# Performance work log

Hardware: AMD Instinct MI355X
Metric: run time of the kernel (lower is better)

Reference implementation:

```python
import jax, jax.numpy as jnp
import numpy as np


def setup_inputs() -> dict:
    key = jax.random.key(0)
    hidden_states = jax.random.normal(key, (8, 4096, 768), dtype=jnp.float32)
    return {"hidden_states": hidden_states}


def reference(hidden_states) -> jnp.ndarray:
    # fft along seq dim (-2), then along hidden dim (-1), keep real part.
    # Equivalent to a 2D FFT over the last two axes.
    x = hidden_states.astype(jnp.float32)
    out = jnp.fft.fft(jnp.fft.fft(x, axis=-2), axis=-1).real
    return out.astype(hidden_states.dtype)
```

## Files before the change

kernel.cpp:

```cpp
#include <hip/hip_runtime.h>
#include <hip/hip_bf16.h>

#define N1 4096
#define N2 768
#define NCC 384
#define WS_NEEDED 100663296ull
#define WS1_UINTS 12582912ull

__device__ __forceinline__ float2 cadd(float2 a, float2 b){ return make_float2(a.x+b.x, a.y+b.y); }
__device__ __forceinline__ float2 csub(float2 a, float2 b){ return make_float2(a.x-b.x, a.y-b.y); }
__device__ __forceinline__ float2 cmul(float2 a, float2 b){ return make_float2(a.x*b.x - a.y*b.y, a.x*b.y + a.y*b.x); }
__device__ __forceinline__ float2 cnegi(float2 a){ return make_float2(a.y, -a.x); }

__device__ __forceinline__ unsigned pack_bf2(float2 v) {
  unsigned ax = __float_as_uint(v.x); ax = (ax + 0x7FFFu + ((ax >> 16) & 1u)) >> 16;
  unsigned ay = __float_as_uint(v.y); ay = (ay + 0x7FFFu + ((ay >> 16) & 1u)) & 0xFFFF0000u;
  return ax | ay;
}
__device__ __forceinline__ float2 unpack_bf2(unsigned u) {
  return make_float2(__uint_as_float(u << 16), __uint_as_float(u & 0xFFFF0000u));
}
__device__ __forceinline__ float bf2f(unsigned short u) {
  return __uint_as_float((unsigned)u << 16);
}

__device__ __forceinline__ int rev6(int p) {
  int k = 0;
  #pragma unroll
  for (int i = 0; i < 6; ++i) { k = (k << 2) | (p & 3); p >>= 2; }
  return k;
}

__device__ __forceinline__ void fft8(float2 z[8]) {
  const float RH = 0.70710678118654752f;
  float2 u0=cadd(z[0],z[4]), v0=csub(z[0],z[4]);
  float2 u1=cadd(z[1],z[5]), v1=csub(z[1],z[5]);
  float2 u2=cadd(z[2],z[6]), v2=csub(z[2],z[6]);
  float2 u3=cadd(z[3],z[7]), v3=csub(z[3],z[7]);
  v1 = make_float2(RH*(v1.x+v1.y), RH*(v1.y-v1.x));
  v2 = cnegi(v2);
  v3 = make_float2(RH*(v3.y-v3.x), -RH*(v3.x+v3.y));
  float2 a0=cadd(u0,u2), b0=csub(u0,u2);
  float2 a1=cadd(u1,u3), b1=cnegi(csub(u1,u3));
  float2 c0=cadd(v0,v2), d0=csub(v0,v2);
  float2 c1=cadd(v1,v3), d1=cnegi(csub(v1,v3));
  z[0]=cadd(a0,a1); z[4]=csub(a0,a1);
  z[2]=cadd(b0,b1); z[6]=csub(b0,b1);
  z[1]=cadd(c0,c1); z[5]=csub(c0,c1);
  z[3]=cadd(d0,d1); z[7]=csub(d0,d1);
}

__global__ __launch_bounds__(1024) void p1a_kernel(const float* __restrict__ x,
                                                   unsigned* __restrict__ ws1) {
  __shared__ float4 S4[64*65];
  float2* S = reinterpret_cast<float2*>(S4);
  int bid = blockIdx.x;
  int b8  = bid & 7;
  int rem = bid >> 3;
  int cg  = rem / 64;
  int a   = rem % 64;
  const int t = threadIdx.x, l = t & 63, w = t >> 6;

  const float* src = x + (size_t)b8 * N1 * N2 + (size_t)cg * 256;
  #pragma unroll
  for (int j = 0; j < 4; ++j) {
    int r   = 4*w + j;
    int row = a + 64*r;
    S4[r*65 + l] = *reinterpret_cast<const float4*>(src + (size_t)row * N2 + 4*l);
  }
  __syncthreads();

  const int c = t & 127, b0 = t >> 7;
  float2 z[8];
  #pragma unroll
  for (int b1 = 0; b1 < 8; ++b1) z[b1] = S[(8*b1 + b0)*130 + c];
  fft8(z);
  {
    float sn, cs; __sincosf(-6.283185307179586f/64.f * (float)b0, &sn, &cs);
    float2 wstep = make_float2(cs, sn), wcur = wstep;
    #pragma unroll
    for (int j = 1; j < 8; ++j) { z[j] = cmul(z[j], wcur); wcur = cmul(wcur, wstep); }
  }
  __syncthreads();
  #pragma unroll
  for (int j = 0; j < 8; ++j) S[(j*8 + b0)*130 + c] = z[j];
  __syncthreads();

  const int jj = t >> 7;
  #pragma unroll
  for (int b0i = 0; b0i < 8; ++b0i) z[b0i] = S[(jj*8 + b0i)*130 + c];
  fft8(z);
  float2 wc, w8;
  { float sn, cs; __sincosf(-6.283185307179586f/4096.f * (float)(a*jj), &sn, &cs); wc = make_float2(cs, sn); }
  { float sn, cs; __sincosf(-6.283185307179586f/4096.f * (float)(8*a),  &sn, &cs); w8 = make_float2(cs, sn); }
  unsigned* wdst = ws1 + (((size_t)b8*64 + a)*3 + cg)*8192 + (size_t)jj*128 + c;
  #pragma unroll
  for (int m = 0; m < 8; ++m) {
    wdst[(size_t)m * 1024] = pack_bf2(cmul(z[m], wc));
    wc = cmul(wc, w8);
  }
}

__global__ __launch_bounds__(1024) void p1b_kernel(const unsigned* __restrict__ ws1,
                                                   unsigned* __restrict__ ws2) {
  __shared__ float2 T[2][4096];
  int bid = blockIdx.x;
  int b8  = bid & 7;
  int rem = bid >> 3;
  int cg  = rem / 32, kbt = rem % 32;
  int kb0 = (kbt == 0) ? 0  : kbt;
  int kb1 = (kbt == 0) ? 32 : 64 - kbt;
  const int t = threadIdx.x, l = t & 63, wv = (t >> 6) & 7, ti = t >> 9;
  const int kb = ti ? kb1 : kb0;
  const int cgA = cg >> 1, chalf = (cg & 1) * 64;

  const unsigned* wsrc = ws1 + ((size_t)b8*64*3 + cgA)*8192
                             + (size_t)kb*128 + chalf + l;
  float2 z[8];
  #pragma unroll
  for (int a1 = 0; a1 < 8; ++a1)
    z[a1] = unpack_bf2(wsrc[(size_t)(8*a1 + wv) * 24576]);
  fft8(z);
  float fac = -6.283185307179586f/64.0f * (float)wv;
  #pragma unroll
  for (int q = 1; q < 8; ++q) {
    float sn, cs; __sincosf(fac * (float)q, &sn, &cs);
    z[q] = cmul(z[q], make_float2(cs, sn));
  }
  #pragma unroll
  for (int q = 0; q < 8; ++q) T[ti][(q*8 + wv)*64 + l] = z[q];
  __syncthreads();
  #pragma unroll
  for (int a0 = 0; a0 < 8; ++a0) z[a0] = T[ti][(wv*8 + a0)*64 + l];
  fft8(z);
  __syncthreads();
  #pragma unroll
  for (int ka1 = 0; ka1 < 8; ++ka1) T[ti][(8*ka1 + wv)*64 + l] = z[ka1];
  __syncthreads();

  unsigned* wout = ws2 + (size_t)b8 * N1 * NCC + (size_t)cg*64 + l;
  #pragma unroll
  for (int it = 0; it < 8; ++it) {
    int ka = 8*it + wv;
    int tj, kap;
    if (kbt == 0) { tj = ti; kap = ti ? (63 - ka) : ((64 - ka) & 63); }
    else          { tj = 1 - ti; kap = 63 - ka; }
    float2 Zk = T[ti][ka*64 + l];
    float2 Zp = T[tj][kap*64 + l];
    int r = kb + 64*ka;
    float2 o;
    if (r <= 2048) o = make_float2(0.5f*(Zk.x + Zp.x), 0.5f*(Zk.y + Zp.y));
    else           o = make_float2(0.5f*(Zp.y - Zk.y), 0.5f*(Zk.x - Zp.x));
    wout[(size_t)r * NCC] = pack_bf2(o);
  }
}

__global__ __launch_bounds__(256) void fft_hid_bf16(const unsigned* __restrict__ ws2,
                                                    float* __restrict__ out) {
  __shared__ float T[4][12*69];
  const int grp = threadIdx.x >> 6;
  const int l   = threadIdx.x & 63;
  int task = blockIdx.x * 4 + grp;
  int b  = task / 2049;
  int t1 = task - b * 2049;
  const bool special = (t1 == 0) || (t1 == 2048);
  const int mrow = special ? t1 : (N1 - t1);
  const unsigned short* pre16 = (const unsigned short*)ws2 + ((size_t)b*N1 + t1)*N2;
  const unsigned short* pim16 = (const unsigned short*)ws2 + ((size_t)b*N1 + mrow)*N2;

  float2 z[12];
  #pragma unroll
  for (int m = 0; m < 12; ++m) {
    float re = bf2f(pre16[(m << 6) + l]);
    float im = special ? 0.0f : bf2f(pim16[(m << 6) + l]);
    z[m] = make_float2(re, im);
  }

  float2 A[3][4];
  #pragma unroll
  for (int q = 0; q < 3; ++q) {
    float2 s0 = z[q], s1 = z[3+q], s2 = z[6+q], s3 = z[9+q];
    float2 t0 = cadd(s0,s2), t1v = csub(s0,s2);
    float2 t2 = cadd(s1,s3), t3 = cnegi(csub(s1,s3));
    A[q][0] = cadd(t0,t2); A[q][1] = cadd(t1v,t3);
    A[q][2] = csub(t0,t2); A[q][3] = csub(t1v,t3);
  }
  const float h3 = 0.8660254037844386f;
  const float2 W1[4] = { {1.f,0.f}, {h3,-0.5f}, {0.5f,-h3}, {0.f,-1.f} };
  const float2 W2[4] = { {1.f,0.f}, {0.5f,-h3}, {-0.5f,-h3}, {-1.f,0.f} };
  float2 y[12];
  #pragma unroll
  for (int k4 = 0; k4 < 4; ++k4) {
    float2 C0 = A[0][k4];
    float2 C1 = cmul(A[1][k4], W1[k4]);
    float2 C2 = cmul(A[2][k4], W2[k4]);
    float2 tt = cadd(C1,C2), d = csub(C1,C2);
    float2 u  = make_float2(C0.x - 0.5f*tt.x, C0.y - 0.5f*tt.y);
    float2 idd = make_float2(h3*d.y, -h3*d.x);
    y[k4]   = cadd(C0, tt);
    y[k4+4] = cadd(u, idd);
    y[k4+8] = csub(u, idd);
  }

  float base = -6.283185307179586f * (float)l / 768.0f;
  #pragma unroll
  for (int km = 1; km < 12; ++km) {
    float sn, cs; __sincosf(base * (float)km, &sn, &cs);
    y[km] = cmul(y[km], make_float2(cs, sn));
  }

  #pragma unroll
  for (int st = 0; st < 6; ++st) {
    int h = 32 >> st;
    int j = l & (h - 1);
    float sn, cs; __sincosf(-3.14159265358979f * (float)j / (float)h, &sn, &cs);
    float2 w = make_float2(cs, sn);
    bool hi = (l & h) != 0;
    #pragma unroll
    for (int m = 0; m < 12; ++m) {
      float px = __shfl_xor(y[m].x, h, 64);
      float py = __shfl_xor(y[m].y, h, 64);
      float2 p = make_float2(px, py);
      float2 lo  = cadd(y[m], p);
      float2 hiv = cmul(csub(p, y[m]), w);
      y[m] = hi ? hiv : lo;
    }
  }

  int r = ((l&1)<<5)|((l&2)<<3)|((l&4)<<1)|((l&8)>>1)|((l&16)>>3)|((l&32)>>5);
  float* Tb = T[grp];
  #pragma unroll
  for (int km = 0; km < 12; ++km) Tb[km*69 + r] = y[km].x;
  __syncthreads();

  float* pre = out + ((size_t)b*N1 + t1)*N2;
  float* pim = out + ((size_t)b*N1 + mrow)*N2;
  #pragma unroll
  for (int mp = 0; mp < 12; ++mp) {
    int k = (mp << 6) + l;
    float v = Tb[(k % 12)*69 + (k / 12)];
    pre[k] = v;
    if (!special) pim[(N2 - k) % N2] = v;
  }
}

#define PADI(i) ((i) + ((i) >> 4))
#define CPBUF 4352

__device__ __forceinline__ void bfly4p(float2* arr, int base, int M, float fac, int np) {
  float2 a0 = arr[PADI(base)], a1 = arr[PADI(base+M)];
  float2 a2 = arr[PADI(base+2*M)], a3 = arr[PADI(base+3*M)];
  float2 t0 = cadd(a0,a2), t1 = csub(a0,a2);
  float2 t2 = cadd(a1,a3), t3 = cnegi(csub(a1,a3));
  float2 y0 = cadd(t0,t2), y1 = cadd(t1,t3), y2 = csub(t0,t2), y3 = csub(t1,t3);
  float ang = fac * (float)np;
  float sn, cs; __sincosf(ang, &sn, &cs);
  float2 w1 = make_float2(cs, sn);
  float2 w2 = cmul(w1,w1);
  float2 w3 = cmul(w2,w1);
  arr[PADI(base)]     = y0;
  arr[PADI(base+M)]   = cmul(y1,w1);
  arr[PADI(base+2*M)] = cmul(y2,w2);
  arr[PADI(base+3*M)] = cmul(y3,w3);
}

__global__ __launch_bounds__(1024) void fft_seq_fused(const float* __restrict__ x,
                                                      float* __restrict__ out) {
  extern __shared__ float2 lds[];
  int bid = blockIdx.x;
  int wg  = (bid & 7) * 96 + (bid >> 3);
  int b   = wg / 96;
  int g   = wg % 96;
  const int t = threadIdx.x;
  const size_t base = (size_t)b * N1 * N2 + 8 * (size_t)g;

  for (int r = t; r < N1; r += 1024) {
    const float* p = x + base + (size_t)r * N2;
    float4 A  = *reinterpret_cast<const float4*>(p);
    float4 Bv = *reinterpret_cast<const float4*>(p + 4);
    int ip = PADI(r);
    lds[ip]             = make_float2(A.x, A.y);
    lds[CPBUF + ip]     = make_float2(A.z, A.w);
    lds[2*CPBUF + ip]   = make_float2(Bv.x, Bv.y);
    lds[3*CPBUF + ip]   = make_float2(Bv.z, Bv.w);
  }
  __syncthreads();

  const int wv  = t >> 6;
  const int cp  = wv & 3;
  const int idx = ((wv >> 2) << 6) + (t & 63);
  float2* buf = lds + cp * CPBUF;

  #pragma unroll
  for (int s = 0; s < 6; ++s) {
    int lm = 10 - 2*s;
    int M  = 1 << lm;
    float fac = -6.283185307179586f / (float)(4*M);
    #pragma unroll
    for (int jj = 0; jj < 4; ++jj) {
      int j   = idx + (jj << 8);
      int np  = j & (M-1);
      int grp = j >> lm;
      int bse = (grp << (lm+2)) + np;
      bfly4p(buf, bse, M, fac, np);
    }
    __syncthreads();
  }

  float* orow = out + base;
  #pragma unroll
  for (int i = 0; i < 4; ++i) {
    int k  = ((t & 63) << 6) + (t >> 6) + (i << 4);
    int km = (N1 - k) & (N1 - 1);
    int pk = PADI(rev6(k));
    int pn = PADI(rev6(km));
    float o[8];
    #pragma unroll
    for (int c = 0; c < 4; ++c) {
      float2 zk = lds[c*CPBUF + pk];
      float2 zn = lds[c*CPBUF + pn];
      if (k <= 2048) { o[2*c] = 0.5f*(zk.x + zn.x); o[2*c+1] = 0.5f*(zk.y + zn.y); }
      else           { o[2*c] = 0.5f*(zn.y - zk.y); o[2*c+1] = 0.5f*(zk.x - zn.x); }
    }
    float* q = orow + (size_t)k * N2;
    *reinterpret_cast<float4*>(q)     = make_float4(o[0], o[1], o[2], o[3]);
    *reinterpret_cast<float4*>(q + 4) = make_float4(o[4], o[5], o[6], o[7]);
  }
}

__global__ __launch_bounds__(256) void fft_hid_f32(float* __restrict__ out) {
  __shared__ float T[4][12*69];
  const int grp = threadIdx.x >> 6;
  const int l   = threadIdx.x & 63;
  int task = blockIdx.x * 4 + grp;
  int b  = task / 2049;
  int t1 = task - b * 2049;
  const bool special = (t1 == 0) || (t1 == 2048);
  const int mrow = special ? t1 : (N1 - t1);
  float* baseB = out + (size_t)b * N1 * N2;
  float* pre = baseB + (size_t)t1 * N2;
  float* pim = baseB + (size_t)mrow * N2;

  float2 z[12];
  #pragma unroll
  for (int m = 0; m < 12; ++m) {
    float re = pre[(m << 6) + l];
    float im = special ? 0.0f : pim[(m << 6) + l];
    z[m] = make_float2(re, im);
  }

  float2 A[3][4];
  #pragma unroll
  for (int q = 0; q < 3; ++q) {
    float2 s0 = z[q], s1 = z[3+q], s2 = z[6+q], s3 = z[9+q];
    float2 t0 = cadd(s0,s2), t1v = csub(s0,s2);
    float2 t2 = cadd(s1,s3), t3 = cnegi(csub(s1,s3));
    A[q][0] = cadd(t0,t2); A[q][1] = cadd(t1v,t3);
    A[q][2] = csub(t0,t2); A[q][3] = csub(t1v,t3);
  }
  const float h3 = 0.8660254037844386f;
  const float2 W1[4] = { {1.f,0.f}, {h3,-0.5f}, {0.5f,-h3}, {0.f,-1.f} };
  const float2 W2[4] = { {1.f,0.f}, {0.5f,-h3}, {-0.5f,-h3}, {-1.f,0.f} };
  float2 y[12];
  #pragma unroll
  for (int k4 = 0; k4 < 4; ++k4) {
    float2 C0 = A[0][k4];
    float2 C1 = cmul(A[1][k4], W1[k4]);
    float2 C2 = cmul(A[2][k4], W2[k4]);
    float2 tt = cadd(C1,C2), d = csub(C1,C2);
    float2 u  = make_float2(C0.x - 0.5f*tt.x, C0.y - 0.5f*tt.y);
    float2 idd = make_float2(h3*d.y, -h3*d.x);
    y[k4]   = cadd(C0, tt);
    y[k4+4] = cadd(u, idd);
    y[k4+8] = csub(u, idd);
  }

  float base = -6.283185307179586f * (float)l / 768.0f;
  #pragma unroll
  for (int km = 1; km < 12; ++km) {
    float sn, cs; __sincosf(base * (float)km, &sn, &cs);
    y[km] = cmul(y[km], make_float2(cs, sn));
  }

  #pragma unroll
  for (int st = 0; st < 6; ++st) {
    int h = 32 >> st;
    int j = l & (h - 1);
    float sn, cs; __sincosf(-3.14159265358979f * (float)j / (float)h, &sn, &cs);
    float2 w = make_float2(cs, sn);
    bool hi = (l & h) != 0;
    #pragma unroll
    for (int m = 0; m < 12; ++m) {
      float px = __shfl_xor(y[m].x, h, 64);
      float py = __shfl_xor(y[m].y, h, 64);
      float2 p = make_float2(px, py);
      float2 lo  = cadd(y[m], p);
      float2 hiv = cmul(csub(p, y[m]), w);
      y[m] = hi ? hiv : lo;
    }
  }

  int r = ((l&1)<<5)|((l&2)<<3)|((l&4)<<1)|((l&8)>>1)|((l&16)>>3)|((l&32)>>5);
  float* Tb = T[grp];
  #pragma unroll
  for (int km = 0; km < 12; ++km) Tb[km*69 + r] = y[km].x;
  __syncthreads();

  #pragma unroll
  for (int mp = 0; mp < 12; ++mp) {
    int k = (mp << 6) + l;
    float v = Tb[(k % 12)*69 + (k / 12)];
    pre[k] = v;
    if (!special) pim[(N2 - k) % N2] = v;
  }
}

extern "C" void kernel_launch(void* const* d_in, const int* in_sizes, int n_in,
                              void* d_out, int out_size, void* d_ws, size_t ws_size,
                              hipStream_t stream) {
  const float* x = (const float*)d_in[0];
  float* out = (float*)d_out;
  if (ws_size >= WS_NEEDED) {
    unsigned* ws1 = (unsigned*)d_ws;
    unsigned* ws2 = ws1 + WS1_UINTS;
    p1a_kernel<<<dim3(1536), dim3(1024), 0, stream>>>(x, ws1);
    p1b_kernel<<<dim3(1536), dim3(1024), 0, stream>>>(ws1, ws2);
    fft_hid_bf16<<<dim3(4098), dim3(256), 0, stream>>>(ws2, out);
  } else {
    (void)hipFuncSetAttribute(reinterpret_cast<const void*>(&fft_seq_fused),
                              hipFuncAttributeMaxDynamicSharedMemorySize,
                              4 * CPBUF * (int)sizeof(float2));
    fft_seq_fused<<<dim3(768), dim3(1024), 4 * CPBUF * sizeof(float2), stream>>>(x, out);
    fft_hid_f32<<<dim3(4098), dim3(256), 0, stream>>>(out);
  }
}
```

Baseline: 94.33 us.

## Make p1a persistent with double-buffered direct global-to-LDS tile loads

The first sequence-FFT kernel now runs 256 blocks that each process 6 tiles in turn, instead of 1536 blocks each doing one tile. The next tile is prefetched into a second LDS buffer with global_load_lds while the current tile is transformed, using manual vmcnt waits and raw barriers. The aim is to hide global load latency behind compute and skip the register round-trip on loads. The cost is fewer resident blocks (133 KB LDS per block) and fragile hand-written waitcnt bookkeeping.

```diff
diff --git a/kernel.cpp b/kernel.cpp
--- a/kernel.cpp
+++ b/kernel.cpp
@@ -6,6 +6,7 @@
 #define NCC 384
 #define WS_NEEDED 100663296ull
 #define WS1_UINTS 12582912ull
+#define TPB_TILES 6
 
 __device__ __forceinline__ float2 cadd(float2 a, float2 b){ return make_float2(a.x+b.x, a.y+b.y); }
 __device__ __forceinline__ float2 csub(float2 a, float2 b){ return make_float2(a.x-b.x, a.y-b.y); }
@@ -52,52 +53,84 @@
 
 __global__ __launch_bounds__(1024) void p1a_kernel(const float* __restrict__ x,
                                                    unsigned* __restrict__ ws1) {
-  __shared__ float4 S4[64*65];
-  float2* S = reinterpret_cast<float2*>(S4);
-  int bid = blockIdx.x;
-  int b8  = bid & 7;
-  int rem = bid >> 3;
-  int cg  = rem / 64;
-  int a   = rem % 64;
+  extern __shared__ float4 S4[];
   const int t = threadIdx.x, l = t & 63, w = t >> 6;
-
-  const float* src = x + (size_t)b8 * N1 * N2 + (size_t)cg * 256;
-  #pragma unroll
-  for (int j = 0; j < 4; ++j) {
-    int r   = 4*w + j;
-    int row = a + 64*r;
-    S4[r*65 + l] = *reinterpret_cast<const float4*>(src + (size_t)row * N2 + 4*l);
-  }
-  __syncthreads();
-
-  const int c = t & 127, b0 = t >> 7;
-  float2 z[8];
-  #pragma unroll
-  for (int b1 = 0; b1 < 8; ++b1) z[b1] = S[(8*b1 + b0)*130 + c];
-  fft8(z);
+  const int tid0 = blockIdx.x * TPB_TILES;
+
   {
-    float sn, cs; __sincosf(-6.283185307179586f/64.f * (float)b0, &sn, &cs);
-    float2 wstep = make_float2(cs, sn), wcur = wstep;
-    #pragma unroll
-    for (int j = 1; j < 8; ++j) { z[j] = cmul(z[j], wcur); wcur = cmul(wcur, wstep); }
-  }
-  __syncthreads();
-  #pragma unroll
-  for (int j = 0; j < 8; ++j) S[(j*8 + b0)*130 + c] = z[j];
-  __syncthreads();
-
-  const int jj = t >> 7;
-  #pragma unroll
-  for (int b0i = 0; b0i < 8; ++b0i) z[b0i] = S[(jj*8 + b0i)*130 + c];
-  fft8(z);
-  float2 wc, w8;
-  { float sn, cs; __sincosf(-6.283185307179586f/4096.f * (float)(a*jj), &sn, &cs); wc = make_float2(cs, sn); }
-  { float sn, cs; __sincosf(-6.283185307179586f/4096.f * (float)(8*a),  &sn, &cs); w8 = make_float2(cs, sn); }
-  unsigned* wdst = ws1 + (((size_t)b8*64 + a)*3 + cg)*8192 + (size_t)jj*128 + c;
-  #pragma unroll
-  for (int m = 0; m < 8; ++m) {
-    wdst[(size_t)m * 1024] = pack_bf2(cmul(z[m], wc));
-    wc = cmul(wc, w8);
+    int tid = tid0;
+    int b8 = tid / 192, r2 = tid % 192, cg = r2 >> 6, a = r2 & 63;
+    const float* src = x + (size_t)b8 * N1 * N2 + (size_t)cg * 256 + 4 * l;
+    #pragma unroll
+    for (int j = 0; j < 4; ++j) {
+      int r = 4 * w + j;
+      __builtin_amdgcn_global_load_lds(
+          (const __attribute__((address_space(1))) unsigned*)(src + (size_t)(a + 64 * r) * N2),
+          (__attribute__((address_space(3))) unsigned*)&S4[r * 65], 16, 0, 0);
+    }
+  }
+
+  #pragma unroll
+  for (int it = 0; it < TPB_TILES; ++it) {
+    const int cur = it & 1;
+    float2* S = reinterpret_cast<float2*>(S4 + cur * 4160);
+
+    if (it + 1 < TPB_TILES) {
+      int tid = tid0 + it + 1;
+      int b8 = tid / 192, r2 = tid % 192, cg = r2 >> 6, a = r2 & 63;
+      const float* src = x + (size_t)b8 * N1 * N2 + (size_t)cg * 256 + 4 * l;
+      #pragma unroll
+      for (int j = 0; j < 4; ++j) {
+        int r = 4 * w + j;
+        __builtin_amdgcn_global_load_lds(
+            (const __attribute__((address_space(1))) unsigned*)(src + (size_t)(a + 64 * r) * N2),
+            (__attribute__((address_space(3))) unsigned*)&S4[(cur ^ 1) * 4160 + r * 65], 16, 0, 0);
+      }
+    }
+
+    if (it == 0)                 asm volatile("s_waitcnt vmcnt(4)" ::: "memory");
+    else if (it + 1 < TPB_TILES) asm volatile("s_waitcnt vmcnt(12)" ::: "memory");
+    else                         asm volatile("s_waitcnt vmcnt(8)" ::: "memory");
+    __builtin_amdgcn_s_barrier();
+
+    int tid = tid0 + it;
+    int r2 = tid % 192;
+    int a  = r2 & 63;
+    int b8 = tid / 192, cg = r2 >> 6;
+
+    const int c = t & 127, b0 = t >> 7;
+    float2 z[8];
+    #pragma unroll
+    for (int b1 = 0; b1 < 8; ++b1) z[b1] = S[(8 * b1 + b0) * 130 + c];
+    fft8(z);
+    {
+      float sn, cs; __sincosf(-6.283185307179586f / 64.f * (float)b0, &sn, &cs);
+      float2 wstep = make_float2(cs, sn), wcur = wstep;
+      #pragma unroll
+      for (int j = 1; j < 8; ++j) { z[j] = cmul(z[j], wcur); wcur = cmul(wcur, wstep); }
+    }
+    asm volatile("s_waitcnt lgkmcnt(0)" ::: "memory");
+    __builtin_amdgcn_s_barrier();
+    #pragma unroll
+    for (int j = 0; j < 8; ++j) S[(j * 8 + b0) * 130 + c] = z[j];
+    asm volatile("s_waitcnt lgkmcnt(0)" ::: "memory");
+    __builtin_amdgcn_s_barrier();
+
+    const int jj = t >> 7;
+    #pragma unroll
+    for (int b0i = 0; b0i < 8; ++b0i) z[b0i] = S[(jj * 8 + b0i) * 130 + c];
+    fft8(z);
+    float2 wc, w8;
+    { float sn, cs; __sincosf(-6.283185307179586f/4096.f * (float)(a * jj), &sn, &cs); wc = make_float2(cs, sn); }
+    { float sn, cs; __sincosf(-6.283185307179586f/4096.f * (float)(8 * a),  &sn, &cs); w8 = make_float2(cs, sn); }
+    unsigned* wdst = ws1 + (((size_t)b8 * 64 + a) * 3 + cg) * 8192 + (size_t)jj * 128 + c;
+    #pragma unroll
+    for (int m = 0; m < 8; ++m) {
+      wdst[(size_t)m * 1024] = pack_bf2(cmul(z[m], wc));
+      wc = cmul(wc, w8);
+    }
+    asm volatile("s_waitcnt lgkmcnt(0)" ::: "memory");
+    __builtin_amdgcn_s_barrier();
   }
 }
 
@@ -423,7 +456,9 @@
   if (ws_size >= WS_NEEDED) {
     unsigned* ws1 = (unsigned*)d_ws;
     unsigned* ws2 = ws1 + WS1_UINTS;
-    p1a_kernel<<<dim3(1536), dim3(1024), 0, stream>>>(x, ws1);
+    (void)hipFuncSetAttribute(reinterpret_cast<const void*>(&p1a_kernel),
+                              hipFuncAttributeMaxDynamicSharedMemorySize, 133120);
+    p1a_kernel<<<dim3(256), dim3(1024), 133120, stream>>>(x, ws1);
     p1b_kernel<<<dim3(1536), dim3(1024), 0, stream>>>(ws1, ws2);
     fft_hid_bf16<<<dim3(4098), dim3(256), 0, stream>>>(ws2, out);
   } else {
```

After: 97.24 us. 3.1% more time.

## Process all three column groups per p1a block with bf16-packed LDS staging

Applied to the files above, without the earlier changes.

The first seq-FFT stage now has each block load full 768-wide rows, pack them to bf16 in a large dynamic LDS buffer, and loop over three column passes. This cuts the grid from 1536 to 512 blocks. The intent is to make row reads fully contiguous and halve LDS footprint per element. In exchange it uses about 129KB of LDS, so only one block fits per CU, and it adds an extra bf16 rounding of the input and of the intermediate values.

```diff
diff --git a/kernel.cpp b/kernel.cpp
--- a/kernel.cpp
+++ b/kernel.cpp
@@ -6,6 +6,7 @@
 #define NCC 384
 #define WS_NEEDED 100663296ull
 #define WS1_UINTS 12582912ull
+#define P1A_LDS 132096
 
 __device__ __forceinline__ float2 cadd(float2 a, float2 b){ return make_float2(a.x+b.x, a.y+b.y); }
 __device__ __forceinline__ float2 csub(float2 a, float2 b){ return make_float2(a.x-b.x, a.y-b.y); }
@@ -52,52 +53,62 @@
 
 __global__ __launch_bounds__(1024) void p1a_kernel(const float* __restrict__ x,
                                                    unsigned* __restrict__ ws1) {
-  __shared__ float4 S4[64*65];
-  float2* S = reinterpret_cast<float2*>(S4);
+  extern __shared__ unsigned LDS[];
+  unsigned* B16 = LDS;
+  unsigned* S16 = LDS + 64*386;
   int bid = blockIdx.x;
-  int b8  = bid & 7;
-  int rem = bid >> 3;
-  int cg  = rem / 64;
-  int a   = rem % 64;
+  int b8 = bid >> 6, a = bid & 63;
   const int t = threadIdx.x, l = t & 63, w = t >> 6;
 
-  const float* src = x + (size_t)b8 * N1 * N2 + (size_t)cg * 256;
+  const float* src = x + ((size_t)b8 * N1 + a) * N2;
   #pragma unroll
   for (int j = 0; j < 4; ++j) {
-    int r   = 4*w + j;
-    int row = a + 64*r;
-    S4[r*65 + l] = *reinterpret_cast<const float4*>(src + (size_t)row * N2 + 4*l);
+    int b = 4*w + j;
+    const float* rp = src + (size_t)(64*b) * N2;
+    float4 v0 = *reinterpret_cast<const float4*>(rp + 4*l);
+    float4 v1 = *reinterpret_cast<const float4*>(rp + 4*(l+64));
+    float4 v2 = *reinterpret_cast<const float4*>(rp + 4*(l+128));
+    unsigned* br = B16 + b*386;
+    *reinterpret_cast<uint2*>(br + 2*l) =
+        make_uint2(pack_bf2(make_float2(v0.x,v0.y)), pack_bf2(make_float2(v0.z,v0.w)));
+    *reinterpret_cast<uint2*>(br + 2*(l+64)) =
+        make_uint2(pack_bf2(make_float2(v1.x,v1.y)), pack_bf2(make_float2(v1.z,v1.w)));
+    *reinterpret_cast<uint2*>(br + 2*(l+128)) =
+        make_uint2(pack_bf2(make_float2(v2.x,v2.y)), pack_bf2(make_float2(v2.z,v2.w)));
   }
   __syncthreads();
 
   const int c = t & 127, b0 = t >> 7;
-  float2 z[8];
-  #pragma unroll
-  for (int b1 = 0; b1 < 8; ++b1) z[b1] = S[(8*b1 + b0)*130 + c];
-  fft8(z);
-  {
-    float sn, cs; __sincosf(-6.283185307179586f/64.f * (float)b0, &sn, &cs);
-    float2 wstep = make_float2(cs, sn), wcur = wstep;
-    #pragma unroll
-    for (int j = 1; j < 8; ++j) { z[j] = cmul(z[j], wcur); wcur = cmul(wcur, wstep); }
-  }
-  __syncthreads();
-  #pragma unroll
-  for (int j = 0; j < 8; ++j) S[(j*8 + b0)*130 + c] = z[j];
-  __syncthreads();
-
-  const int jj = t >> 7;
-  #pragma unroll
-  for (int b0i = 0; b0i < 8; ++b0i) z[b0i] = S[(jj*8 + b0i)*130 + c];
-  fft8(z);
-  float2 wc, w8;
-  { float sn, cs; __sincosf(-6.283185307179586f/4096.f * (float)(a*jj), &sn, &cs); wc = make_float2(cs, sn); }
-  { float sn, cs; __sincosf(-6.283185307179586f/4096.f * (float)(8*a),  &sn, &cs); w8 = make_float2(cs, sn); }
-  unsigned* wdst = ws1 + (((size_t)b8*64 + a)*3 + cg)*8192 + (size_t)jj*128 + c;
-  #pragma unroll
-  for (int m = 0; m < 8; ++m) {
-    wdst[(size_t)m * 1024] = pack_bf2(cmul(z[m], wc));
-    wc = cmul(wc, w8);
+  for (int pass = 0; pass < 3; ++pass) {
+    float2 z[8];
+    #pragma unroll
+    for (int b1 = 0; b1 < 8; ++b1)
+      z[b1] = unpack_bf2(B16[(8*b1 + b0)*386 + pass*128 + c]);
+    fft8(z);
+    {
+      float sn, cs; __sincosf(-6.283185307179586f/64.f * (float)b0, &sn, &cs);
+      float2 wstep = make_float2(cs, sn), wcur = wstep;
+      #pragma unroll
+      for (int j = 1; j < 8; ++j) { z[j] = cmul(z[j], wcur); wcur = cmul(wcur, wstep); }
+    }
+    __syncthreads();
+    #pragma unroll
+    for (int j = 0; j < 8; ++j) S16[(j*8 + b0)*130 + c] = pack_bf2(z[j]);
+    __syncthreads();
+
+    const int jj = b0;
+    #pragma unroll
+    for (int i = 0; i < 8; ++i) z[i] = unpack_bf2(S16[(jj*8 + i)*130 + c]);
+    fft8(z);
+    float2 wc, w8;
+    { float sn, cs; __sincosf(-6.283185307179586f/4096.f * (float)(a*jj), &sn, &cs); wc = make_float2(cs, sn); }
+    { float sn, cs; __sincosf(-6.283185307179586f/4096.f * (float)(8*a),  &sn, &cs); w8 = make_float2(cs, sn); }
+    unsigned* wdst = ws1 + (((size_t)b8*64 + a)*3 + pass)*8192 + (size_t)jj*128 + c;
+    #pragma unroll
+    for (int m = 0; m < 8; ++m) {
+      wdst[(size_t)m * 1024] = pack_bf2(cmul(z[m], wc));
+      wc = cmul(wc, w8);
+    }
   }
 }
 
@@ -423,7 +434,9 @@
   if (ws_size >= WS_NEEDED) {
     unsigned* ws1 = (unsigned*)d_ws;
     unsigned* ws2 = ws1 + WS1_UINTS;
-    p1a_kernel<<<dim3(1536), dim3(1024), 0, stream>>>(x, ws1);
+    (void)hipFuncSetAttribute(reinterpret_cast<const void*>(&p1a_kernel),
+                              hipFuncAttributeMaxDynamicSharedMemorySize, P1A_LDS);
+    p1a_kernel<<<dim3(512), dim3(1024), P1A_LDS, stream>>>(x, ws1);
     p1b_kernel<<<dim3(1536), dim3(1024), 0, stream>>>(ws1, ws2);
     fft_hid_bf16<<<dim3(4098), dim3(256), 0, stream>>>(ws2, out);
   } else {
```

Measured after the change: 99.44 us. 1.05x slower.

## Compute first-pass 64-point FFT per thread in registers instead of shared memory

Applied to the files above, without the earlier changes.

The first sequence-FFT stage now has each thread load 64 strided complex values into registers and do both radix-8 passes locally, with no shared-memory transposes or block barriers. Blocks shrink to 256 threads, and each wave handles one (batch, row-offset, column-chunk) job. This removes LDS traffic and synchronisation, but uses a large register array per thread, which cuts occupancy. The global loads also become 8-byte accesses with a large row stride, where the old code did coalesced float4 loads.

```diff
diff --git a/kernel.cpp b/kernel.cpp
--- a/kernel.cpp
+++ b/kernel.cpp
@@ -50,54 +50,51 @@
   z[3]=cadd(d0,d1); z[7]=csub(d0,d1);
 }
 
-__global__ __launch_bounds__(1024) void p1a_kernel(const float* __restrict__ x,
-                                                   unsigned* __restrict__ ws1) {
-  __shared__ float4 S4[64*65];
-  float2* S = reinterpret_cast<float2*>(S4);
-  int bid = blockIdx.x;
-  int b8  = bid & 7;
-  int rem = bid >> 3;
-  int cg  = rem / 64;
-  int a   = rem % 64;
+__global__ __launch_bounds__(256) void p1a_kernel(const float* __restrict__ x,
+                                                  unsigned* __restrict__ ws1) {
   const int t = threadIdx.x, l = t & 63, w = t >> 6;
-
-  const float* src = x + (size_t)b8 * N1 * N2 + (size_t)cg * 256;
-  #pragma unroll
-  for (int j = 0; j < 4; ++j) {
-    int r   = 4*w + j;
-    int row = a + 64*r;
-    S4[r*65 + l] = *reinterpret_cast<const float4*>(src + (size_t)row * N2 + 4*l);
-  }
-  __syncthreads();
-
-  const int c = t & 127, b0 = t >> 7;
-  float2 z[8];
-  #pragma unroll
-  for (int b1 = 0; b1 < 8; ++b1) z[b1] = S[(8*b1 + b0)*130 + c];
-  fft8(z);
-  {
-    float sn, cs; __sincosf(-6.283185307179586f/64.f * (float)b0, &sn, &cs);
+  int job = blockIdx.x * 4 + w;
+  int b8  = job / 384;
+  int rem = job - b8 * 384;
+  int a   = rem / 6;
+  int cw  = rem - a * 6;
+
+  const float* src = x + ((size_t)(b8 * N1 + a)) * N2 + 2 * (cw * 64 + l);
+  float2 Z[64];
+  #pragma unroll
+  for (int b = 0; b < 64; ++b)
+    Z[b] = *reinterpret_cast<const float2*>(src + (size_t)b * 64 * N2);
+
+  #pragma unroll
+  for (int b0 = 0; b0 < 8; ++b0) {
+    float2 tt[8];
+    #pragma unroll
+    for (int b1 = 0; b1 < 8; ++b1) tt[b1] = Z[8 * b1 + b0];
+    fft8(tt);
+    float sn, cs; __sincosf(-6.283185307179586f / 64.f * (float)b0, &sn, &cs);
     float2 wstep = make_float2(cs, sn), wcur = wstep;
     #pragma unroll
-    for (int j = 1; j < 8; ++j) { z[j] = cmul(z[j], wcur); wcur = cmul(wcur, wstep); }
-  }
-  __syncthreads();
-  #pragma unroll
-  for (int j = 0; j < 8; ++j) S[(j*8 + b0)*130 + c] = z[j];
-  __syncthreads();
-
-  const int jj = t >> 7;
-  #pragma unroll
-  for (int b0i = 0; b0i < 8; ++b0i) z[b0i] = S[(jj*8 + b0i)*130 + c];
-  fft8(z);
-  float2 wc, w8;
-  { float sn, cs; __sincosf(-6.283185307179586f/4096.f * (float)(a*jj), &sn, &cs); wc = make_float2(cs, sn); }
-  { float sn, cs; __sincosf(-6.283185307179586f/4096.f * (float)(8*a),  &sn, &cs); w8 = make_float2(cs, sn); }
-  unsigned* wdst = ws1 + (((size_t)b8*64 + a)*3 + cg)*8192 + (size_t)jj*128 + c;
-  #pragma unroll
-  for (int m = 0; m < 8; ++m) {
-    wdst[(size_t)m * 1024] = pack_bf2(cmul(z[m], wc));
-    wc = cmul(wc, w8);
+    for (int k0 = 1; k0 < 8; ++k0) { tt[k0] = cmul(tt[k0], wcur); wcur = cmul(wcur, wstep); }
+    #pragma unroll
+    for (int k0 = 0; k0 < 8; ++k0) Z[k0 * 8 + b0] = tt[k0];
+  }
+
+  unsigned* wdst = ws1 + (((size_t)b8 * 64 + a) * 3 + (cw >> 1)) * 8192
+                       + (size_t)((cw & 1) * 64 + l);
+  #pragma unroll
+  for (int jj = 0; jj < 8; ++jj) {
+    float2 tt[8];
+    #pragma unroll
+    for (int b0 = 0; b0 < 8; ++b0) tt[b0] = Z[jj * 8 + b0];
+    fft8(tt);
+    float2 wc, w8;
+    { float sn, cs; __sincosf(-6.283185307179586f/4096.f * (float)(a * jj), &sn, &cs); wc = make_float2(cs, sn); }
+    { float sn, cs; __sincosf(-6.283185307179586f/4096.f * (float)(8 * a),  &sn, &cs); w8 = make_float2(cs, sn); }
+    #pragma unroll
+    for (int m = 0; m < 8; ++m) {
+      wdst[(size_t)(8 * m + jj) * 128] = pack_bf2(cmul(tt[m], wc));
+      wc = cmul(wc, w8);
+    }
   }
 }
 
@@ -423,7 +420,7 @@
   if (ws_size >= WS_NEEDED) {
     unsigned* ws1 = (unsigned*)d_ws;
     unsigned* ws2 = ws1 + WS1_UINTS;
-    p1a_kernel<<<dim3(1536), dim3(1024), 0, stream>>>(x, ws1);
+    p1a_kernel<<<dim3(768), dim3(256), 0, stream>>>(x, ws1);
     p1b_kernel<<<dim3(1536), dim3(1024), 0, stream>>>(ws1, ws2);
     fft_hid_bf16<<<dim3(4098), dim3(256), 0, stream>>>(ws2, out);
   } else {
```

Result: no change. 95.47 us (+1.2%).
